# Performance work log

Measured on AMD Instinct MI355X. Metric: run time of the kernel, lower is better.

The kernel has to match this reference:

```python
import jax, jax.numpy as jnp
import numpy as np

LN_EPS = 1e-5  # torch.nn.LayerNorm default

QLEN, MLEN, BATCH, D_MODEL = 1024, 1024, 8, 1024


def _ft_matrix(qlen, klen):
    """Real part of the causal Fourier matrix (imag part never contributes:
    the input is real and the module takes .real of the product)."""
    ft_len = klen - qlen + 1
    m = jnp.arange(qlen, dtype=jnp.float32)
    k = jnp.arange(ft_len, dtype=jnp.float32)
    base = jnp.cos((2.0 * float(np.pi)) * jnp.outer(m, k) / float(ft_len))
    base = base / float(np.sqrt(ft_len))                      # [qlen, ft_len]
    mat = jnp.pad(base, ((0, 0), (klen - ft_len, 0)))          # left-pad -> [qlen, klen]
    # row i rolled left by (qlen - 1 - i), vectorized as a gather
    shift = (qlen - 1) - jnp.arange(qlen)                      # [qlen]
    cols = (jnp.arange(klen)[None, :] + shift[:, None]) % klen  # [qlen, klen]
    mat = jnp.take_along_axis(mat, cols, axis=1)
    rows = jnp.arange(qlen)[:, None]
    js = jnp.arange(klen)[None, :]
    # tril(diagonal=klen-qlen) AND triu(0)  (same_length=True)
    mask = (js <= rows + (klen - qlen)) & (js >= rows)
    return jnp.where(mask, mat, jnp.float32(0.0))


def setup_inputs() -> dict:
    key = jax.random.key(0)
    k1, k2, k3 = jax.random.split(key, 3)
    return {
        "dec_inp": jax.random.normal(k1, (QLEN, BATCH, D_MODEL), dtype=jnp.float32),
        "pos_emb": jax.random.normal(k2, (QLEN + MLEN, 1, D_MODEL), dtype=jnp.float32),
        "mems": jax.random.normal(k3, (MLEN, BATCH, D_MODEL), dtype=jnp.float32),
        "gamma": jnp.ones((D_MODEL,), dtype=jnp.float32),
        "beta": jnp.zeros((D_MODEL,), dtype=jnp.float32),
        "add_position": 1,
    }


def reference(dec_inp, pos_emb, mems, gamma, beta, add_position):
    qlen = dec_inp.shape[0]
    klen = qlen + mems.shape[0]
    cat = jnp.concatenate([mems, dec_inp], axis=0)  # [klen, b, d]
    if add_position:
        cat = cat + pos_emb  # dropout is identity in eval mode
    ft_mat = _ft_matrix(qlen, klen)                 # [qlen, klen]
    ft = jnp.einsum('ml,lbd->mbd', ft_mat, cat)     # real part of complex matmul
    x = dec_inp + ft / float(np.sqrt(klen))
    mu = jnp.mean(x, axis=-1, keepdims=True)
    var = jnp.var(x, axis=-1, keepdims=True)
    return gamma * (x - mu) * jax.lax.rsqrt(var + LN_EPS) + beta
```

## Files before the change

### kernel.cpp

```cpp
#include <hip/hip_runtime.h>
#include <hip/hip_bf16.h>

#define QLEN   1024
#define MLEN   1024
#define KLEN   2048
#define BATCH  8
#define DMODEL 1024
#define NCOLS  (BATCH * DMODEL)
#define FTLEN  1025

#define BM 128
#define BN 256
#define BK 64
#define NT 18

typedef __attribute__((ext_vector_type(4))) float f32x4;
typedef __attribute__((ext_vector_type(8))) short bf16x8;

typedef __attribute__((address_space(1))) const unsigned int as1_u32;
typedef __attribute__((address_space(3))) unsigned int as3_u32;

static __device__ __forceinline__ unsigned short f2bf(float f) {
    unsigned int u = __builtin_bit_cast(unsigned int, f);
    return (unsigned short)((u + 0x7fffu + ((u >> 16) & 1u)) >> 16);
}
static __device__ __forceinline__ float bf2f(unsigned short s) {
    return __builtin_bit_cast(float, (unsigned int)s << 16);
}
static __device__ __forceinline__ unsigned int packbf(float lo, float hi) {
    return (unsigned int)f2bf(lo) | ((unsigned int)f2bf(hi) << 16);
}

__global__ __launch_bounds__(256) void prep_transpose2(
    const float* __restrict__ dec, const float* __restrict__ pos,
    const float* __restrict__ mems, const int* __restrict__ addp,
    unsigned short* __restrict__ catT)
{
    __shared__ unsigned int T2[32 * 68];
    const int tid = threadIdx.x;
    const int lt = blockIdx.x, dt = blockIdx.y, b = blockIdx.z;
    const int l0 = lt * 64, d0 = dt * 64;
    const int add_position = addp[0];

    const int dloc  = (tid & 15) * 4;
    const int lhalf = tid >> 4;

    float4 vc[2][2];
#pragma unroll
    for (int p = 0; p < 2; ++p)
#pragma unroll
        for (int jl = 0; jl < 2; ++jl) {
            const int l = l0 + p * 32 + lhalf * 2 + jl;
            const float* src = (l < MLEN)
                ? (mems + (size_t)l * NCOLS + b * DMODEL + d0 + dloc)
                : (dec + (size_t)(l - MLEN) * NCOLS + b * DMODEL + d0 + dloc);
            vc[p][jl] = *reinterpret_cast<const float4*>(src);
        }
    if (add_position) {
#pragma unroll
        for (int p = 0; p < 2; ++p)
#pragma unroll
            for (int jl = 0; jl < 2; ++jl) {
                const int l = l0 + p * 32 + lhalf * 2 + jl;
                float4 pv = *reinterpret_cast<const float4*>(
                    pos + (size_t)l * DMODEL + d0 + dloc);
                vc[p][jl].x += pv.x; vc[p][jl].y += pv.y;
                vc[p][jl].z += pv.z; vc[p][jl].w += pv.w;
            }
    }
#pragma unroll
    for (int p = 0; p < 2; ++p) {
        const int lp = p * 16 + lhalf;
        uint4 w;
        w.x = packbf(vc[p][0].x, vc[p][1].x);
        w.y = packbf(vc[p][0].y, vc[p][1].y);
        w.z = packbf(vc[p][0].z, vc[p][1].z);
        w.w = packbf(vc[p][0].w, vc[p][1].w);
        *reinterpret_cast<uint4*>(&T2[lp * 68 + dloc]) = w;
    }
    __syncthreads();
    const int d = tid >> 2;
    const size_t n = (size_t)b * DMODEL + d0 + d;
#pragma unroll
    for (int q = 0; q < 2; ++q) {
        const int c8 = (tid & 3) + 4 * q;
        uint4 o;
        o.x = T2[(c8 * 4 + 0) * 68 + d];
        o.y = T2[(c8 * 4 + 1) * 68 + d];
        o.z = T2[(c8 * 4 + 2) * 68 + d];
        o.w = T2[(c8 * 4 + 3) * 68 + d];
        *reinterpret_cast<uint4*>(&catT[n * KLEN + l0 + c8 * 8]) = o;
    }
}

__global__ __launch_bounds__(256) void fill_w(unsigned short* __restrict__ W)
{
    const int idx = blockIdx.x * 256 + threadIdx.x;
    const int m = idx >> 9;
    const int k4 = (idx & 511) * 4;
    union { unsigned short s[4]; int2 v; } u;
    for (int j = 0; j < 4; ++j) {
        const int k = k4 + j;
        const int t = k - m;
        float w = 0.0f;
        if (t >= 0 && t < FTLEN) {
            const int r = (m * t) % FTLEN;
            const float x = (float)r * (1.0f / (float)FTLEN);
            float c;
            asm("v_cos_f32 %0, %1" : "=v"(c) : "v"(x));
            w = c * 0.03123475237772121f;
        }
        u.s[j] = f2bf(w);
    }
    *reinterpret_cast<int2*>(&W[(size_t)m * KLEN + k4]) = u.v;
}

__global__ __launch_bounds__(512) void gemm_band4(
    const unsigned short* __restrict__ W,
    const unsigned short* __restrict__ catT,
    unsigned short* __restrict__ ftout)
{
    __shared__ unsigned short Alds[3][BM * BK];
    __shared__ unsigned short Blds[3][BN * BK];

    const int tid = threadIdx.x;
    const int wave = tid >> 6, lane = tid & 63;

    const int bid = blockIdx.x;
    const int xcd = bid & 7;
    const int kk = bid >> 3;
    const int m_idx = kk >> 2;
    const int n_idx = xcd * 4 + (kk & 3);
    const int m0 = m_idx * BM, n0 = n_idx * BN;
    const int wm = wave >> 2, wn = wave & 3;

    f32x4 acc[4][4];
    for (int i = 0; i < 4; ++i)
        for (int j = 0; j < 4; ++j)
            acc[i][j] = (f32x4){0.f, 0.f, 0.f, 0.f};

    const int srow = tid >> 3;
    const int scol = (((tid & 7) ^ ((tid >> 3) & 7)) * 8);
    const int fr = lane & 15;
    const int kg = lane >> 4;
    const int rswz = (fr & 7) * 8;

#define STAGE_LOAD_A(S, T, P) do {                                              \
    const int k0_ = m0 + (T) * BK;                                              \
    const int row = (P) * 64 + srow;                                            \
    __builtin_amdgcn_global_load_lds(                                           \
        (as1_u32*)(const void*)(W + (size_t)(m0 + row) * KLEN + k0_ + scol),    \
        (as3_u32*)(void*)(&Alds[S][row * BK + scol]), 16, 0, 0);                \
} while (0)
#define STAGE_LOAD_B(S, T, P) do {                                              \
    const int k0_ = m0 + (T) * BK;                                              \
    const int row = (P) * 64 + srow;                                            \
    __builtin_amdgcn_global_load_lds(                                           \
        (as1_u32*)(const void*)(catT + (size_t)(n0 + row) * KLEN + k0_ + scol), \
        (as3_u32*)(void*)(&Blds[S][row * BK + scol]), 16, 0, 0);                \
} while (0)
#define STAGE_ALL(S, T) do {                                                    \
    STAGE_LOAD_A(S, T, 0); STAGE_LOAD_A(S, T, 1);                               \
    STAGE_LOAD_B(S, T, 0); STAGE_LOAD_B(S, T, 1);                               \
    STAGE_LOAD_B(S, T, 2); STAGE_LOAD_B(S, T, 3);                               \
} while (0)

    STAGE_ALL(0, 0);
    STAGE_ALL(1, 1);

    for (int t = 0; t < NT; ++t) {
        if (t == NT - 1)
            asm volatile("s_waitcnt vmcnt(0)" ::: "memory");
        else
            asm volatile("s_waitcnt vmcnt(6)" ::: "memory");
        __builtin_amdgcn_s_barrier();

        const unsigned short* Ab = Alds[t % 3];
        const unsigned short* Bb = Blds[t % 3];
        const int s2 = (t + 2) % 3;
        const bool pf = (t + 2 < NT);

        {
            bf16x8 a[4], b[4];
#pragma unroll
            for (int f = 0; f < 4; ++f)
                a[f] = *reinterpret_cast<const bf16x8*>(
                    Ab + (wm * 64 + f * 16 + fr) * BK + ((kg * 8) ^ rswz));
#pragma unroll
            for (int f = 0; f < 4; ++f)
                b[f] = *reinterpret_cast<const bf16x8*>(
                    Bb + (wn * 64 + f * 16 + fr) * BK + ((kg * 8) ^ rswz));
            if (pf) { STAGE_LOAD_A(s2, t + 2, 0); STAGE_LOAD_B(s2, t + 2, 0); STAGE_LOAD_B(s2, t + 2, 1); }
            __builtin_amdgcn_s_barrier();
            asm volatile("s_waitcnt lgkmcnt(0)" ::: "memory");
            __builtin_amdgcn_s_setprio(1);
#pragma unroll
            for (int fm = 0; fm < 4; ++fm)
#pragma unroll
                for (int fn = 0; fn < 4; ++fn)
                    acc[fm][fn] = __builtin_amdgcn_mfma_f32_16x16x32_bf16(
                        a[fm], b[fn], acc[fm][fn], 0, 0, 0);
            __builtin_amdgcn_s_setprio(0);
            __builtin_amdgcn_s_barrier();
        }
        {
            bf16x8 a[4], b[4];
#pragma unroll
            for (int f = 0; f < 4; ++f)
                a[f] = *reinterpret_cast<const bf16x8*>(
                    Ab + (wm * 64 + f * 16 + fr) * BK + ((32 + kg * 8) ^ rswz));
#pragma unroll
            for (int f = 0; f < 4; ++f)
                b[f] = *reinterpret_cast<const bf16x8*>(
                    Bb + (wn * 64 + f * 16 + fr) * BK + ((32 + kg * 8) ^ rswz));
            if (pf) { STAGE_LOAD_A(s2, t + 2, 1); STAGE_LOAD_B(s2, t + 2, 2); STAGE_LOAD_B(s2, t + 2, 3); }
            __builtin_amdgcn_s_barrier();
            asm volatile("s_waitcnt lgkmcnt(0)" ::: "memory");
            __builtin_amdgcn_s_setprio(1);
#pragma unroll
            for (int fm = 0; fm < 4; ++fm)
#pragma unroll
                for (int fn = 0; fn < 4; ++fn)
                    acc[fm][fn] = __builtin_amdgcn_mfma_f32_16x16x32_bf16(
                        a[fm], b[fn], acc[fm][fn], 0, 0, 0);
            __builtin_amdgcn_s_setprio(0);
        }
    }
#undef STAGE_ALL
#undef STAGE_LOAD_A
#undef STAGE_LOAD_B

    const int col16 = lane & 15, rquad = lane >> 4;
#pragma unroll
    for (int fm = 0; fm < 4; ++fm)
#pragma unroll
        for (int fn = 0; fn < 4; ++fn)
#pragma unroll
            for (int j = 0; j < 4; ++j) {
                const int m = m0 + wm * 64 + fm * 16 + rquad * 4 + j;
                const int n = n0 + wn * 64 + fn * 16 + col16;
                ftout[(size_t)m * NCOLS + n] = f2bf(acc[fm][fn][j]);
            }
}

__global__ __launch_bounds__(256) void layernorm_rows(
    const unsigned short* __restrict__ ft, const float* __restrict__ dec,
    const float* __restrict__ gamma, const float* __restrict__ beta,
    float* __restrict__ out)
{
    __shared__ float ps[4], pq[4];
    const int row = blockIdx.x;
    const int tid = threadIdx.x;
    const float inv = 0.022097086912079612f;
    const size_t base = (size_t)row * DMODEL + tid * 4;
    ushort4 u = *reinterpret_cast<const ushort4*>(ft + base);
    float4 dv = *reinterpret_cast<const float4*>(dec + base);
    float vx = dv.x + bf2f(u.x) * inv;
    float vy = dv.y + bf2f(u.y) * inv;
    float vz = dv.z + bf2f(u.z) * inv;
    float vw = dv.w + bf2f(u.w) * inv;
    float s  = vx + vy + vz + vw;
    float sq = vx * vx + vy * vy + vz * vz + vw * vw;
    for (int off = 32; off > 0; off >>= 1) {
        s  += __shfl_down(s, off);
        sq += __shfl_down(sq, off);
    }
    const int wave = tid >> 6, lane = tid & 63;
    if (lane == 0) { ps[wave] = s; pq[wave] = sq; }
    __syncthreads();
    if (tid == 0) {
        float ts = ps[0] + ps[1] + ps[2] + ps[3];
        float tq = pq[0] + pq[1] + pq[2] + pq[3];
        float mu = ts * (1.0f / DMODEL);
        float var = tq * (1.0f / DMODEL) - mu * mu;
        ps[0] = mu;
        pq[0] = rsqrtf(var + 1e-5f);
    }
    __syncthreads();
    const float mu = ps[0], rs = pq[0];
    float4 g  = *reinterpret_cast<const float4*>(gamma + tid * 4);
    float4 be = *reinterpret_cast<const float4*>(beta + tid * 4);
    float4 o;
    o.x = g.x * (vx - mu) * rs + be.x;
    o.y = g.y * (vy - mu) * rs + be.y;
    o.z = g.z * (vz - mu) * rs + be.z;
    o.w = g.w * (vw - mu) * rs + be.w;
    *reinterpret_cast<float4*>(out + base) = o;
}

extern "C" void kernel_launch(void* const* d_in, const int* in_sizes, int n_in,
                              void* d_out, int out_size, void* d_ws, size_t ws_size,
                              hipStream_t stream)
{
    const float* dec   = (const float*)d_in[0];
    const float* pos   = (const float*)d_in[1];
    const float* mems  = (const float*)d_in[2];
    const float* gamma = (const float*)d_in[3];
    const float* beta  = (const float*)d_in[4];
    const int*   addp  = (const int*)d_in[5];
    float* out = (float*)d_out;

    unsigned short* catT = (unsigned short*)d_ws;
    unsigned short* Wmat = catT + (size_t)NCOLS * KLEN;
    unsigned short* ft   = Wmat + (size_t)QLEN * KLEN;

    prep_transpose2<<<dim3(32, 16, 8), 256, 0, stream>>>(dec, pos, mems, addp, catT);
    fill_w<<<2048, 256, 0, stream>>>(Wmat);
    gemm_band4<<<256, 512, 0, stream>>>(Wmat, catT, ft);
    layernorm_rows<<<8192, 256, 0, stream>>>(ft, dec, gamma, beta, out);
}
```

Measured before the change: 64.13 us.

## Generate Fourier weight tiles in-register inside GEMM instead of separate fill kernel

```diff
diff --git a/kernel.cpp b/kernel.cpp
--- a/kernel.cpp
+++ b/kernel.cpp
@@ -29,6 +29,13 @@
 }
 static __device__ __forceinline__ unsigned int packbf(float lo, float hi) {
     return (unsigned int)f2bf(lo) | ((unsigned int)f2bf(hi) << 16);
+}
+static __device__ __forceinline__ unsigned mod1025(unsigned x) {
+    unsigned q = (unsigned)((float)x * (1.0f / 1025.0f));
+    int r = (int)x - (int)(q * 1025u);
+    if (r < 0) r += 1025;
+    if (r >= 1025) r -= 1025;
+    return (unsigned)r;
 }
 
 __global__ __launch_bounds__(256) void prep_transpose2(
@@ -93,30 +100,7 @@
     }
 }
 
-__global__ __launch_bounds__(256) void fill_w(unsigned short* __restrict__ W)
-{
-    const int idx = blockIdx.x * 256 + threadIdx.x;
-    const int m = idx >> 9;
-    const int k4 = (idx & 511) * 4;
-    union { unsigned short s[4]; int2 v; } u;
-    for (int j = 0; j < 4; ++j) {
-        const int k = k4 + j;
-        const int t = k - m;
-        float w = 0.0f;
-        if (t >= 0 && t < FTLEN) {
-            const int r = (m * t) % FTLEN;
-            const float x = (float)r * (1.0f / (float)FTLEN);
-            float c;
-            asm("v_cos_f32 %0, %1" : "=v"(c) : "v"(x));
-            w = c * 0.03123475237772121f;
-        }
-        u.s[j] = f2bf(w);
-    }
-    *reinterpret_cast<int2*>(&W[(size_t)m * KLEN + k4]) = u.v;
-}
-
-__global__ __launch_bounds__(512) void gemm_band4(
-    const unsigned short* __restrict__ W,
+__global__ __launch_bounds__(512) void gemm_band5(
     const unsigned short* __restrict__ catT,
     unsigned short* __restrict__ ftout)
 {
@@ -140,39 +124,68 @@
             acc[i][j] = (f32x4){0.f, 0.f, 0.f, 0.f};
 
     const int srow = tid >> 3;
+    const int kcol = (tid & 7) * 8;
     const int scol = (((tid & 7) ^ ((tid >> 3) & 7)) * 8);
     const int fr = lane & 15;
     const int kg = lane >> 4;
     const int rswz = (fr & 7) * 8;
 
-#define STAGE_LOAD_A(S, T, P) do {                                              \
-    const int k0_ = m0 + (T) * BK;                                              \
-    const int row = (P) * 64 + srow;                                            \
-    __builtin_amdgcn_global_load_lds(                                           \
-        (as1_u32*)(const void*)(W + (size_t)(m0 + row) * KLEN + k0_ + scol),    \
-        (as3_u32*)(void*)(&Alds[S][row * BK + scol]), 16, 0, 0);                \
+    unsigned mlane[2], c64g[2], rgen[2];
+    int ttgen[2];
+#pragma unroll
+    for (int P = 0; P < 2; ++P) {
+        const int row = P * 64 + srow;
+        const unsigned m = (unsigned)(m0 + row);
+        mlane[P] = m;
+        c64g[P] = mod1025(64u * m);
+        const int tt0 = kcol - row;
+        ttgen[P] = tt0;
+        const unsigned tmod = (unsigned)(tt0 < 0 ? tt0 + 1025 : tt0);
+        rgen[P] = mod1025(m * tmod);
+    }
+
+#define GEN_W(S, P) do {                                                        \
+    unsigned r_ = rgen[P]; int tt_ = ttgen[P];                                  \
+    const unsigned m_ = mlane[P];                                               \
+    float f_[8];                                                                \
+    _Pragma("unroll")                                                           \
+    for (int j = 0; j < 8; ++j) {                                               \
+        float c_;                                                               \
+        asm("v_cos_f32 %0, %1" : "=v"(c_)                                       \
+            : "v"((float)r_ * (1.0f / 1025.0f)));                               \
+        f_[j] = (tt_ >= 0 && tt_ < FTLEN) ? c_ * 0.03123475237772121f : 0.0f;   \
+        r_ += m_; if (r_ >= 1025u) r_ -= 1025u;                                 \
+        ++tt_;                                                                  \
+    }                                                                           \
+    uint4 wv_;                                                                  \
+    asm("v_cvt_pk_bf16_f32 %0, %1, %2" : "=v"(wv_.x) : "v"(f_[0]), "v"(f_[1]));\
+    asm("v_cvt_pk_bf16_f32 %0, %1, %2" : "=v"(wv_.y) : "v"(f_[2]), "v"(f_[3]));\
+    asm("v_cvt_pk_bf16_f32 %0, %1, %2" : "=v"(wv_.z) : "v"(f_[4]), "v"(f_[5]));\
+    asm("v_cvt_pk_bf16_f32 %0, %1, %2" : "=v"(wv_.w) : "v"(f_[6]), "v"(f_[7]));\
+    *reinterpret_cast<uint4*>(&Alds[S][((P) * 64 + srow) * BK + scol]) = wv_;   \
+    rgen[P] += c64g[P]; if (rgen[P] >= 1025u) rgen[P] -= 1025u;                 \
+    ttgen[P] += 64;                                                             \
 } while (0)
-#define STAGE_LOAD_B(S, T, P) do {                                              \
+
+#define STAGE_B(S, T, P) do {                                                   \
     const int k0_ = m0 + (T) * BK;                                              \
     const int row = (P) * 64 + srow;                                            \
     __builtin_amdgcn_global_load_lds(                                           \
         (as1_u32*)(const void*)(catT + (size_t)(n0 + row) * KLEN + k0_ + scol), \
         (as3_u32*)(void*)(&Blds[S][row * BK + scol]), 16, 0, 0);                \
 } while (0)
-#define STAGE_ALL(S, T) do {                                                    \
-    STAGE_LOAD_A(S, T, 0); STAGE_LOAD_A(S, T, 1);                               \
-    STAGE_LOAD_B(S, T, 0); STAGE_LOAD_B(S, T, 1);                               \
-    STAGE_LOAD_B(S, T, 2); STAGE_LOAD_B(S, T, 3);                               \
-} while (0)
-
-    STAGE_ALL(0, 0);
-    STAGE_ALL(1, 1);
+
+    STAGE_B(0, 0, 0); STAGE_B(0, 0, 1); STAGE_B(0, 0, 2); STAGE_B(0, 0, 3);
+    STAGE_B(1, 1, 0); STAGE_B(1, 1, 1); STAGE_B(1, 1, 2); STAGE_B(1, 1, 3);
+    GEN_W(0, 0); GEN_W(0, 1);
+    GEN_W(1, 0); GEN_W(1, 1);
+    asm volatile("s_waitcnt lgkmcnt(0)" ::: "memory");
 
     for (int t = 0; t < NT; ++t) {
         if (t == NT - 1)
             asm volatile("s_waitcnt vmcnt(0)" ::: "memory");
         else
-            asm volatile("s_waitcnt vmcnt(6)" ::: "memory");
+            asm volatile("s_waitcnt vmcnt(4)" ::: "memory");
         __builtin_amdgcn_s_barrier();
 
         const unsigned short* Ab = Alds[t % 3];
@@ -190,7 +203,7 @@
             for (int f = 0; f < 4; ++f)
                 b[f] = *reinterpret_cast<const bf16x8*>(
                     Bb + (wn * 64 + f * 16 + fr) * BK + ((kg * 8) ^ rswz));
-            if (pf) { STAGE_LOAD_A(s2, t + 2, 0); STAGE_LOAD_B(s2, t + 2, 0); STAGE_LOAD_B(s2, t + 2, 1); }
+            if (pf) { STAGE_B(s2, t + 2, 0); STAGE_B(s2, t + 2, 1); GEN_W(s2, 0); }
             __builtin_amdgcn_s_barrier();
             asm volatile("s_waitcnt lgkmcnt(0)" ::: "memory");
             __builtin_amdgcn_s_setprio(1);
@@ -213,7 +226,7 @@
             for (int f = 0; f < 4; ++f)
                 b[f] = *reinterpret_cast<const bf16x8*>(
                     Bb + (wn * 64 + f * 16 + fr) * BK + ((32 + kg * 8) ^ rswz));
-            if (pf) { STAGE_LOAD_A(s2, t + 2, 1); STAGE_LOAD_B(s2, t + 2, 2); STAGE_LOAD_B(s2, t + 2, 3); }
+            if (pf) { STAGE_B(s2, t + 2, 2); STAGE_B(s2, t + 2, 3); GEN_W(s2, 1); }
             __builtin_amdgcn_s_barrier();
             asm volatile("s_waitcnt lgkmcnt(0)" ::: "memory");
             __builtin_amdgcn_s_setprio(1);
@@ -226,9 +239,8 @@
             __builtin_amdgcn_s_setprio(0);
         }
     }
-#undef STAGE_ALL
-#undef STAGE_LOAD_A
-#undef STAGE_LOAD_B
+#undef STAGE_B
+#undef GEN_W
 
     const int col16 = lane & 15, rquad = lane >> 4;
 #pragma unroll
@@ -301,11 +313,9 @@
     float* out = (float*)d_out;
 
     unsigned short* catT = (unsigned short*)d_ws;
-    unsigned short* Wmat = catT + (size_t)NCOLS * KLEN;
-    unsigned short* ft   = Wmat + (size_t)QLEN * KLEN;
+    unsigned short* ft   = catT + (size_t)NCOLS * KLEN;
 
     prep_transpose2<<<dim3(32, 16, 8), 256, 0, stream>>>(dec, pos, mems, addp, catT);
-    fill_w<<<2048, 256, 0, stream>>>(Wmat);
-    gemm_band4<<<256, 512, 0, stream>>>(Wmat, catT, ft);
+    gemm_band5<<<256, 512, 0, stream>>>(catT, ft);
     layernorm_rows<<<8192, 256, 0, stream>>>(ft, dec, gamma, beta, out);
 }
```

Result: slower. 69.64 us (+8.6%).

## Shrink GEMM tiles to 128x128x32 with 4-stage LDS pipeline and single barrier

Applied to the files above, without the earlier changes.

```diff
diff --git a/kernel.cpp b/kernel.cpp
--- a/kernel.cpp
+++ b/kernel.cpp
@@ -10,9 +10,10 @@
 #define FTLEN  1025
 
 #define BM 128
-#define BN 256
-#define BK 64
-#define NT 18
+#define BN 128
+#define BK 32
+#define NT 36
+#define NBUF 4
 
 typedef __attribute__((ext_vector_type(4))) float f32x4;
 typedef __attribute__((ext_vector_type(8))) short bf16x8;
@@ -115,13 +116,13 @@
     *reinterpret_cast<int2*>(&W[(size_t)m * KLEN + k4]) = u.v;
 }
 
-__global__ __launch_bounds__(512) void gemm_band4(
+__global__ __launch_bounds__(512) void gemm_band7(
     const unsigned short* __restrict__ W,
     const unsigned short* __restrict__ catT,
     unsigned short* __restrict__ ftout)
 {
-    __shared__ unsigned short Alds[3][BM * BK];
-    __shared__ unsigned short Blds[3][BN * BK];
+    __shared__ unsigned short Alds[NBUF][BM * BK];
+    __shared__ unsigned short Blds[NBUF][BN * BK];
 
     const int tid = threadIdx.x;
     const int wave = tid >> 6, lane = tid & 63;
@@ -129,116 +130,82 @@
     const int bid = blockIdx.x;
     const int xcd = bid & 7;
     const int kk = bid >> 3;
-    const int m_idx = kk >> 2;
-    const int n_idx = xcd * 4 + (kk & 3);
+    const int m_idx = kk >> 3;
+    const int n_idx = xcd * 8 + (kk & 7);
     const int m0 = m_idx * BM, n0 = n_idx * BN;
     const int wm = wave >> 2, wn = wave & 3;
 
-    f32x4 acc[4][4];
+    f32x4 acc[4][2];
+#pragma unroll
     for (int i = 0; i < 4; ++i)
-        for (int j = 0; j < 4; ++j)
+#pragma unroll
+        for (int j = 0; j < 2; ++j)
             acc[i][j] = (f32x4){0.f, 0.f, 0.f, 0.f};
 
-    const int srow = tid >> 3;
-    const int scol = (((tid & 7) ^ ((tid >> 3) & 7)) * 8);
+    const int srow = tid >> 2;
+    const int scol = (tid & 3) * 8;
     const int fr = lane & 15;
     const int kg = lane >> 4;
-    const int rswz = (fr & 7) * 8;
-
-#define STAGE_LOAD_A(S, T, P) do {                                              \
+
+#define STAGE(S, T) do {                                                        \
     const int k0_ = m0 + (T) * BK;                                              \
-    const int row = (P) * 64 + srow;                                            \
     __builtin_amdgcn_global_load_lds(                                           \
-        (as1_u32*)(const void*)(W + (size_t)(m0 + row) * KLEN + k0_ + scol),    \
-        (as3_u32*)(void*)(&Alds[S][row * BK + scol]), 16, 0, 0);                \
+        (as1_u32*)(const void*)(W + (size_t)(m0 + srow) * KLEN + k0_ + scol),   \
+        (as3_u32*)(void*)(&Alds[S][srow * BK + scol]), 16, 0, 0);               \
+    __builtin_amdgcn_global_load_lds(                                           \
+        (as1_u32*)(const void*)(catT + (size_t)(n0 + srow) * KLEN + k0_ + scol),\
+        (as3_u32*)(void*)(&Blds[S][srow * BK + scol]), 16, 0, 0);               \
 } while (0)
-#define STAGE_LOAD_B(S, T, P) do {                                              \
-    const int k0_ = m0 + (T) * BK;                                              \
-    const int row = (P) * 64 + srow;                                            \
-    __builtin_amdgcn_global_load_lds(                                           \
-        (as1_u32*)(const void*)(catT + (size_t)(n0 + row) * KLEN + k0_ + scol), \
-        (as3_u32*)(void*)(&Blds[S][row * BK + scol]), 16, 0, 0);                \
-} while (0)
-#define STAGE_ALL(S, T) do {                                                    \
-    STAGE_LOAD_A(S, T, 0); STAGE_LOAD_A(S, T, 1);                               \
-    STAGE_LOAD_B(S, T, 0); STAGE_LOAD_B(S, T, 1);                               \
-    STAGE_LOAD_B(S, T, 2); STAGE_LOAD_B(S, T, 3);                               \
-} while (0)
-
-    STAGE_ALL(0, 0);
-    STAGE_ALL(1, 1);
+
+    STAGE(0, 0);
+    STAGE(1, 1);
+    STAGE(2, 2);
 
     for (int t = 0; t < NT; ++t) {
-        if (t == NT - 1)
+        if (t < NT - 2)
+            asm volatile("s_waitcnt vmcnt(4)" ::: "memory");
+        else if (t == NT - 2)
+            asm volatile("s_waitcnt vmcnt(2)" ::: "memory");
+        else
             asm volatile("s_waitcnt vmcnt(0)" ::: "memory");
-        else
-            asm volatile("s_waitcnt vmcnt(6)" ::: "memory");
         __builtin_amdgcn_s_barrier();
 
-        const unsigned short* Ab = Alds[t % 3];
-        const unsigned short* Bb = Blds[t % 3];
-        const int s2 = (t + 2) % 3;
-        const bool pf = (t + 2 < NT);
-
-        {
-            bf16x8 a[4], b[4];
-#pragma unroll
-            for (int f = 0; f < 4; ++f)
-                a[f] = *reinterpret_cast<const bf16x8*>(
-                    Ab + (wm * 64 + f * 16 + fr) * BK + ((kg * 8) ^ rswz));
-#pragma unroll
-            for (int f = 0; f < 4; ++f)
-                b[f] = *reinterpret_cast<const bf16x8*>(
-                    Bb + (wn * 64 + f * 16 + fr) * BK + ((kg * 8) ^ rswz));
-            if (pf) { STAGE_LOAD_A(s2, t + 2, 0); STAGE_LOAD_B(s2, t + 2, 0); STAGE_LOAD_B(s2, t + 2, 1); }
-            __builtin_amdgcn_s_barrier();
-            asm volatile("s_waitcnt lgkmcnt(0)" ::: "memory");
-            __builtin_amdgcn_s_setprio(1);
-#pragma unroll
-            for (int fm = 0; fm < 4; ++fm)
-#pragma unroll
-                for (int fn = 0; fn < 4; ++fn)
-                    acc[fm][fn] = __builtin_amdgcn_mfma_f32_16x16x32_bf16(
-                        a[fm], b[fn], acc[fm][fn], 0, 0, 0);
-            __builtin_amdgcn_s_setprio(0);
-            __builtin_amdgcn_s_barrier();
-        }
-        {
-            bf16x8 a[4], b[4];
-#pragma unroll
-            for (int f = 0; f < 4; ++f)
-                a[f] = *reinterpret_cast<const bf16x8*>(
-                    Ab + (wm * 64 + f * 16 + fr) * BK + ((32 + kg * 8) ^ rswz));
-#pragma unroll
-            for (int f = 0; f < 4; ++f)
-                b[f] = *reinterpret_cast<const bf16x8*>(
-                    Bb + (wn * 64 + f * 16 + fr) * BK + ((32 + kg * 8) ^ rswz));
-            if (pf) { STAGE_LOAD_A(s2, t + 2, 1); STAGE_LOAD_B(s2, t + 2, 2); STAGE_LOAD_B(s2, t + 2, 3); }
-            __builtin_amdgcn_s_barrier();
-            asm volatile("s_waitcnt lgkmcnt(0)" ::: "memory");
-            __builtin_amdgcn_s_setprio(1);
-#pragma unroll
-            for (int fm = 0; fm < 4; ++fm)
-#pragma unroll
-                for (int fn = 0; fn < 4; ++fn)
-                    acc[fm][fn] = __builtin_amdgcn_mfma_f32_16x16x32_bf16(
-                        a[fm], b[fn], acc[fm][fn], 0, 0, 0);
-            __builtin_amdgcn_s_setprio(0);
-        }
-    }
-#undef STAGE_ALL
-#undef STAGE_LOAD_A
-#undef STAGE_LOAD_B
+        const unsigned short* Ab = Alds[t & 3];
+        const unsigned short* Bb = Blds[t & 3];
+
+        bf16x8 a[4], b[2];
+#pragma unroll
+        for (int f = 0; f < 4; ++f)
+            a[f] = *reinterpret_cast<const bf16x8*>(
+                Ab + (wm * 64 + f * 16 + fr) * BK + kg * 8);
+#pragma unroll
+        for (int f = 0; f < 2; ++f)
+            b[f] = *reinterpret_cast<const bf16x8*>(
+                Bb + (wn * 32 + f * 16 + fr) * BK + kg * 8);
+
+        if (t + 3 < NT) STAGE((t + 3) & 3, t + 3);
+
+        asm volatile("s_waitcnt lgkmcnt(0)" ::: "memory");
+        __builtin_amdgcn_s_setprio(1);
+#pragma unroll
+        for (int fm = 0; fm < 4; ++fm)
+#pragma unroll
+            for (int fn = 0; fn < 2; ++fn)
+                acc[fm][fn] = __builtin_amdgcn_mfma_f32_16x16x32_bf16(
+                    a[fm], b[fn], acc[fm][fn], 0, 0, 0);
+        __builtin_amdgcn_s_setprio(0);
+    }
+#undef STAGE
 
     const int col16 = lane & 15, rquad = lane >> 4;
 #pragma unroll
     for (int fm = 0; fm < 4; ++fm)
 #pragma unroll
-        for (int fn = 0; fn < 4; ++fn)
+        for (int fn = 0; fn < 2; ++fn)
 #pragma unroll
             for (int j = 0; j < 4; ++j) {
                 const int m = m0 + wm * 64 + fm * 16 + rquad * 4 + j;
-                const int n = n0 + wn * 64 + fn * 16 + col16;
+                const int n = n0 + wn * 32 + fn * 16 + col16;
                 ftout[(size_t)m * NCOLS + n] = f2bf(acc[fm][fn][j]);
             }
 }
@@ -306,6 +273,6 @@
 
     prep_transpose2<<<dim3(32, 16, 8), 256, 0, stream>>>(dec, pos, mems, addp, catT);
     fill_w<<<2048, 256, 0, stream>>>(Wmat);
-    gemm_band4<<<256, 512, 0, stream>>>(Wmat, catT, ft);
+    gemm_band7<<<512, 512, 0, stream>>>(Wmat, catT, ft);
     layernorm_rows<<<8192, 256, 0, stream>>>(ft, dec, gamma, beta, out);
 }
```

New measurement: 65.69 us. +2.4%, slower.

## Load A operand directly from global into registers, bypassing LDS

Applied to the files above, without the earlier changes.

```diff
diff --git a/kernel.cpp b/kernel.cpp
--- a/kernel.cpp
+++ b/kernel.cpp
@@ -115,12 +115,11 @@
     *reinterpret_cast<int2*>(&W[(size_t)m * KLEN + k4]) = u.v;
 }
 
-__global__ __launch_bounds__(512) void gemm_band4(
+__global__ __launch_bounds__(512) void gemm_band8(
     const unsigned short* __restrict__ W,
     const unsigned short* __restrict__ catT,
     unsigned short* __restrict__ ftout)
 {
-    __shared__ unsigned short Alds[3][BM * BK];
     __shared__ unsigned short Blds[3][BN * BK];
 
     const int tid = threadIdx.x;
@@ -145,90 +144,101 @@
     const int kg = lane >> 4;
     const int rswz = (fr & 7) * 8;
 
-#define STAGE_LOAD_A(S, T, P) do {                                              \
-    const int k0_ = m0 + (T) * BK;                                              \
-    const int row = (P) * 64 + srow;                                            \
-    __builtin_amdgcn_global_load_lds(                                           \
-        (as1_u32*)(const void*)(W + (size_t)(m0 + row) * KLEN + k0_ + scol),    \
-        (as3_u32*)(void*)(&Alds[S][row * BK + scol]), 16, 0, 0);                \
+    const unsigned short* pA0 = W + (size_t)(m0 + wm * 64 + 0 * 16 + fr) * KLEN + m0 + kg * 8;
+    const unsigned short* pA1 = W + (size_t)(m0 + wm * 64 + 1 * 16 + fr) * KLEN + m0 + kg * 8;
+    const unsigned short* pA2 = W + (size_t)(m0 + wm * 64 + 2 * 16 + fr) * KLEN + m0 + kg * 8;
+    const unsigned short* pA3 = W + (size_t)(m0 + wm * 64 + 3 * 16 + fr) * KLEN + m0 + kg * 8;
+
+    bf16x8 aA[2][4], aB[2][4];
+
+#define LOAD_A_KS(AN, KS) do {                                                  \
+    AN[KS][0] = *reinterpret_cast<const bf16x8*>(pA0 + (KS) * 32);              \
+    AN[KS][1] = *reinterpret_cast<const bf16x8*>(pA1 + (KS) * 32);              \
+    AN[KS][2] = *reinterpret_cast<const bf16x8*>(pA2 + (KS) * 32);              \
+    AN[KS][3] = *reinterpret_cast<const bf16x8*>(pA3 + (KS) * 32);              \
 } while (0)
-#define STAGE_LOAD_B(S, T, P) do {                                              \
+#define ADV_A() do { pA0 += BK; pA1 += BK; pA2 += BK; pA3 += BK; } while (0)
+
+#define STAGE_B(S, T, P) do {                                                   \
     const int k0_ = m0 + (T) * BK;                                              \
     const int row = (P) * 64 + srow;                                            \
     __builtin_amdgcn_global_load_lds(                                           \
         (as1_u32*)(const void*)(catT + (size_t)(n0 + row) * KLEN + k0_ + scol), \
         (as3_u32*)(void*)(&Blds[S][row * BK + scol]), 16, 0, 0);                \
 } while (0)
-#define STAGE_ALL(S, T) do {                                                    \
-    STAGE_LOAD_A(S, T, 0); STAGE_LOAD_A(S, T, 1);                               \
-    STAGE_LOAD_B(S, T, 0); STAGE_LOAD_B(S, T, 1);                               \
-    STAGE_LOAD_B(S, T, 2); STAGE_LOAD_B(S, T, 3);                               \
+
+    STAGE_B(0, 0, 0); STAGE_B(0, 0, 1); STAGE_B(0, 0, 2); STAGE_B(0, 0, 3);
+    LOAD_A_KS(aA, 0);
+    STAGE_B(1, 1, 0); STAGE_B(1, 1, 1);
+    LOAD_A_KS(aA, 1);
+    STAGE_B(1, 1, 2); STAGE_B(1, 1, 3);
+    ADV_A();
+
+#define ITER(T, AC, AN) do {                                                    \
+                         \
+    if ((T) == NT - 1) asm volatile("s_waitcnt vmcnt(8)" ::: "memory");         \
+    else               asm volatile("s_waitcnt vmcnt(12)" ::: "memory");        \
+    __builtin_amdgcn_s_barrier();                                               \
+    const unsigned short* Bb = Blds[(T) % 3];                                   \
+    const int s2_ = ((T) + 2) % 3;                                              \
+    const bool pfA = (T) + 1 < NT, pfB = (T) + 2 < NT;                          \
+                                                  \
+    {                                                                           \
+        bf16x8 b[4];                                                            \
+        _Pragma("unroll")                                                       \
+        for (int f = 0; f < 4; ++f)                                             \
+            b[f] = *reinterpret_cast<const bf16x8*>(                            \
+                Bb + (wn * 64 + f * 16 + fr) * BK + ((kg * 8) ^ rswz));         \
+        if (pfA) LOAD_A_KS(AN, 0);                                              \
+        if (pfB) { STAGE_B(s2_, (T) + 2, 0); STAGE_B(s2_, (T) + 2, 1); }        \
+        __builtin_amdgcn_s_barrier();                                           \
+        if ((T) == NT - 1)                                                      \
+            asm volatile("s_waitcnt vmcnt(0) lgkmcnt(0)" ::: "memory");         \
+        else if ((T) == NT - 2)                                                 \
+            asm volatile("s_waitcnt vmcnt(6) lgkmcnt(0)" ::: "memory");         \
+        else                                                                    \
+            asm volatile("s_waitcnt vmcnt(8) lgkmcnt(0)" ::: "memory");         \
+        __builtin_amdgcn_s_setprio(1);                                          \
+        _Pragma("unroll")                                                       \
+        for (int fm = 0; fm < 4; ++fm)                                          \
+            _Pragma("unroll")                                                   \
+            for (int fn = 0; fn < 4; ++fn)                                      \
+                acc[fm][fn] = __builtin_amdgcn_mfma_f32_16x16x32_bf16(          \
+                    AC[0][fm], b[fn], acc[fm][fn], 0, 0, 0);                    \
+        __builtin_amdgcn_s_setprio(0);                                          \
+        __builtin_amdgcn_s_barrier();                                           \
+    }                                                                           \
+                                                  \
+    {                                                                           \
+        bf16x8 b[4];                                                            \
+        _Pragma("unroll")                                                       \
+        for (int f = 0; f < 4; ++f)                                             \
+            b[f] = *reinterpret_cast<const bf16x8*>(                            \
+                Bb + (wn * 64 + f * 16 + fr) * BK + ((32 + kg * 8) ^ rswz));    \
+        if (pfA) LOAD_A_KS(AN, 1);                                              \
+        if (pfB) { STAGE_B(s2_, (T) + 2, 2); STAGE_B(s2_, (T) + 2, 3); }        \
+        __builtin_amdgcn_s_barrier();                                           \
+        asm volatile("s_waitcnt lgkmcnt(0)" ::: "memory");                      \
+        __builtin_amdgcn_s_setprio(1);                                          \
+        _Pragma("unroll")                                                       \
+        for (int fm = 0; fm < 4; ++fm)                                          \
+            _Pragma("unroll")                                                   \
+            for (int fn = 0; fn < 4; ++fn)                                      \
+                acc[fm][fn] = __builtin_amdgcn_mfma_f32_16x16x32_bf16(          \
+                    AC[1][fm], b[fn], acc[fm][fn], 0, 0, 0);                    \
+        __builtin_amdgcn_s_setprio(0);                                          \
+    }                                                                           \
+    ADV_A();                                                                    \
 } while (0)
 
-    STAGE_ALL(0, 0);
-    STAGE_ALL(1, 1);
-
-    for (int t = 0; t < NT; ++t) {
-        if (t == NT - 1)
-            asm volatile("s_waitcnt vmcnt(0)" ::: "memory");
-        else
-            asm volatile("s_waitcnt vmcnt(6)" ::: "memory");
-        __builtin_amdgcn_s_barrier();
-
-        const unsigned short* Ab = Alds[t % 3];
-        const unsigned short* Bb = Blds[t % 3];
-        const int s2 = (t + 2) % 3;
-        const bool pf = (t + 2 < NT);
-
-        {
-            bf16x8 a[4], b[4];
-#pragma unroll
-            for (int f = 0; f < 4; ++f)
-                a[f] = *reinterpret_cast<const bf16x8*>(
-                    Ab + (wm * 64 + f * 16 + fr) * BK + ((kg * 8) ^ rswz));
-#pragma unroll
-            for (int f = 0; f < 4; ++f)
-                b[f] = *reinterpret_cast<const bf16x8*>(
-                    Bb + (wn * 64 + f * 16 + fr) * BK + ((kg * 8) ^ rswz));
-            if (pf) { STAGE_LOAD_A(s2, t + 2, 0); STAGE_LOAD_B(s2, t + 2, 0); STAGE_LOAD_B(s2, t + 2, 1); }
-            __builtin_amdgcn_s_barrier();
-            asm volatile("s_waitcnt lgkmcnt(0)" ::: "memory");
-            __builtin_amdgcn_s_setprio(1);
-#pragma unroll
-            for (int fm = 0; fm < 4; ++fm)
-#pragma unroll
-                for (int fn = 0; fn < 4; ++fn)
-                    acc[fm][fn] = __builtin_amdgcn_mfma_f32_16x16x32_bf16(
-                        a[fm], b[fn], acc[fm][fn], 0, 0, 0);
-            __builtin_amdgcn_s_setprio(0);
-            __builtin_amdgcn_s_barrier();
-        }
-        {
-            bf16x8 a[4], b[4];
-#pragma unroll
-            for (int f = 0; f < 4; ++f)
-                a[f] = *reinterpret_cast<const bf16x8*>(
-                    Ab + (wm * 64 + f * 16 + fr) * BK + ((32 + kg * 8) ^ rswz));
-#pragma unroll
-            for (int f = 0; f < 4; ++f)
-                b[f] = *reinterpret_cast<const bf16x8*>(
-                    Bb + (wn * 64 + f * 16 + fr) * BK + ((32 + kg * 8) ^ rswz));
-            if (pf) { STAGE_LOAD_A(s2, t + 2, 1); STAGE_LOAD_B(s2, t + 2, 2); STAGE_LOAD_B(s2, t + 2, 3); }
-            __builtin_amdgcn_s_barrier();
-            asm volatile("s_waitcnt lgkmcnt(0)" ::: "memory");
-            __builtin_amdgcn_s_setprio(1);
-#pragma unroll
-            for (int fm = 0; fm < 4; ++fm)
-#pragma unroll
-                for (int fn = 0; fn < 4; ++fn)
-                    acc[fm][fn] = __builtin_amdgcn_mfma_f32_16x16x32_bf16(
-                        a[fm], b[fn], acc[fm][fn], 0, 0, 0);
-            __builtin_amdgcn_s_setprio(0);
-        }
-    }
-#undef STAGE_ALL
-#undef STAGE_LOAD_A
-#undef STAGE_LOAD_B
+    for (int tt = 0; tt < NT / 2; ++tt) {
+        ITER(2 * tt,     aA, aB);
+        ITER(2 * tt + 1, aB, aA);
+    }
+#undef ITER
+#undef STAGE_B
+#undef LOAD_A_KS
+#undef ADV_A
 
     const int col16 = lane & 15, rquad = lane >> 4;
 #pragma unroll
@@ -306,6 +316,6 @@
 
     prep_transpose2<<<dim3(32, 16, 8), 256, 0, stream>>>(dec, pos, mems, addp, catT);
     fill_w<<<2048, 256, 0, stream>>>(Wmat);
-    gemm_band4<<<256, 512, 0, stream>>>(Wmat, catT, ft);
+    gemm_band8<<<256, 512, 0, stream>>>(Wmat, catT, ft);
     layernorm_rows<<<8192, 256, 0, stream>>>(ft, dec, gamma, beta, out);
 }
```

New measurement: 87.31 us. 36.1% more time.
